# Kernel optimization log

Measured on AMD Instinct MI355X. Metric: run time of the kernel, lower is better.

Reference implementation:

```python
import jax, jax.numpy as jnp
import numpy as np

B, S, D_IN, D_OUT, H = 2, 2048, 1024, 1024, 16
HD = D_OUT // H

def setup_inputs() -> dict:
    key = jax.random.key(0)
    ks = jax.random.split(key, 6)
    sc = 1.0 / np.sqrt(D_IN)
    return {
        "x": jax.random.normal(ks[0], (B, S, D_IN), dtype=jnp.float32),
        "Wq": jax.random.normal(ks[1], (D_IN, D_OUT), dtype=jnp.float32) * sc,
        "Wk": jax.random.normal(ks[2], (D_IN, D_OUT), dtype=jnp.float32) * sc,
        "Wv": jax.random.normal(ks[3], (D_IN, D_OUT), dtype=jnp.float32) * sc,
        "Wo": jax.random.normal(ks[4], (D_OUT, D_OUT), dtype=jnp.float32) * (1.0 / np.sqrt(D_OUT)),
        "bo": jax.random.normal(ks[5], (D_OUT,), dtype=jnp.float32) * 0.01,
    }

def reference(x, Wq, Wk, Wv, Wo, bo):
    b, n, _ = x.shape
    # QKV projections -> [b, h, n, hd]
    def split_heads(t):
        return t.reshape(b, n, H, HD).transpose(0, 2, 1, 3)
    q = split_heads(x @ Wq)
    k = split_heads(x @ Wk)
    v = split_heads(x @ Wv)
    scores = jnp.einsum("bhqd,bhkd->bhqk", q, k) / jnp.sqrt(jnp.float32(HD))
    causal = jnp.tril(jnp.ones((n, n), dtype=bool))  # True = keep
    scores = jnp.where(causal[None, None], scores, -jnp.inf)
    attn = jax.nn.softmax(scores, axis=-1)
    ctx = jnp.einsum("bhqk,bhkd->bhqd", attn, v)  # [b,h,n,hd]
    ctx = ctx.transpose(0, 2, 1, 3).reshape(b, n, D_OUT)
    return ctx @ Wo + bo
```

## Files before the change

kernel.cpp:

```cpp
#include <hip/hip_runtime.h>

#define B_  2
#define S_  2048
#define D_  1024
#define H_  16
#define HD_ 64
#define M_  (B_*S_)

typedef __bf16 bf16_t;
typedef __bf16 bf16x8 __attribute__((ext_vector_type(8)));
typedef float  f32x4  __attribute__((ext_vector_type(4)));

union U16x8 { uint4 u; bf16x8 v; };
union U16x4 { uint2 u; bf16_t e[4]; };

__device__ __forceinline__ bf16x8 ld_frag(const bf16_t* p) {
    U16x8 t; t.u = *(const uint4*)p; return t.v;
}

__device__ __forceinline__ void gload16(const bf16_t* g, bf16_t* l) {
    __builtin_amdgcn_global_load_lds(
        (const __attribute__((address_space(1))) unsigned int*)g,
        (__attribute__((address_space(3))) unsigned int*)l,
        16, 0, 0);
}

__global__ __launch_bounds__(256) void ingest(const float* __restrict__ w0,
                                              const float* __restrict__ w1,
                                              const float* __restrict__ w2,
                                              const float* __restrict__ w3,
                                              const float* __restrict__ xin,
                                              bf16_t* __restrict__ wtout,
                                              bf16_t* __restrict__ xout) {
    const int RC = 1024;
    int z = blockIdx.z;
    if (z == 4) {
        int bid = blockIdx.y * 32 + blockIdx.x;
        int t = threadIdx.y * 32 + threadIdx.x;
        int i = bid * 4096 + t * 16;
#pragma unroll
        for (int g = 0; g < 2; g++) {
            float4 a = *(const float4*)(xin + i + g * 8);
            float4 b = *(const float4*)(xin + i + g * 8 + 4);
            bf16_t o[8] = {(bf16_t)a.x, (bf16_t)a.y, (bf16_t)a.z, (bf16_t)a.w,
                           (bf16_t)b.x, (bf16_t)b.y, (bf16_t)b.z, (bf16_t)b.w};
            *(uint4*)(xout + i + g * 8) = *(uint4*)o;
        }
        return;
    }
    __shared__ bf16_t tile[32][33];
    const float* in = (z == 0) ? w0 : (z == 1) ? w1 : (z == 2) ? w2 : w3;
    bf16_t* out = wtout + (size_t)z * RC * RC;
    int c0 = blockIdx.x * 32, r0 = blockIdx.y * 32;
    int tx = threadIdx.x, ty = threadIdx.y;
#pragma unroll
    for (int i = 0; i < 32; i += 8)
        tile[ty + i][tx] = (bf16_t)in[(size_t)(r0 + ty + i) * RC + c0 + tx];
    __syncthreads();
#pragma unroll
    for (int i = 0; i < 32; i += 8)
        out[(size_t)(c0 + ty + i) * RC + r0 + tx] = tile[tx][ty + i];
}

#define STAGE_TILE(A_, Wt_, koff, buf)                                        \
    _Pragma("unroll") for (int c = 0; c < 4; c++) {                           \
        int rb = c * 32 + wid * 8;                                            \
        gload16(A_  + arow + (size_t)rb * K + (koff), (buf) + rb * 64);       \
        gload16(Wt_ + brow + (size_t)rb * K + (koff), (buf) + 8192 + rb * 64);\
    }

#define GEMM_CORE(A_, Wt_)                                                    \
    const int K = 1024;                                                       \
    __shared__ __align__(16) bf16_t smem[32768];                              \
    int t = threadIdx.x;                                                      \
    int wid = t >> 6, lane = t & 63, ln = lane & 15, quad = lane >> 4;        \
    int wm = (wid >> 1) * 64, wn = (wid & 1) * 64;                            \
    f32x4 zero = {0.f, 0.f, 0.f, 0.f};                                        \
    f32x4 acc[4][4];                                                          \
    _Pragma("unroll") for (int i = 0; i < 4; i++)                             \
        _Pragma("unroll") for (int j = 0; j < 4; j++) acc[i][j] = zero;       \
    int sr8 = lane >> 3;                                                      \
    int scs = (((lane & 7) ^ sr8) * 8);              \
    int swr = (ln & 7) * 8;                          \
    const size_t arow = (size_t)(m0 + sr8) * K + scs;                         \
    const size_t brow = (size_t)(n0 + sr8) * K + scs;                         \
    STAGE_TILE(A_, Wt_, 0, smem)                                              \
    STAGE_TILE(A_, Wt_, 64, smem + 16384)                                     \
    for (int it = 0; it < 16; it++) {                                         \
        if (it < 15) asm volatile("s_waitcnt vmcnt(8)" ::: "memory");         \
        else         asm volatile("s_waitcnt vmcnt(0)" ::: "memory");         \
        __builtin_amdgcn_sched_barrier(0);                                    \
        __builtin_amdgcn_s_barrier();                                         \
        bf16_t* a_lds = smem + (it & 1) * 16384;                              \
        bf16_t* b_lds = a_lds + 8192;                                         \
        _Pragma("unroll") for (int ks = 0; ks < 2; ks++) {                    \
            bf16x8 af[4], bfr[4];                                             \
            _Pragma("unroll") for (int i = 0; i < 4; i++)                     \
                af[i] = ld_frag(a_lds + (wm + i * 16 + ln) * 64 +             \
                                ((ks * 32 + quad * 8) ^ swr));                \
            _Pragma("unroll") for (int j = 0; j < 4; j++)                     \
                bfr[j] = ld_frag(b_lds + (wn + j * 16 + ln) * 64 +            \
                                 ((ks * 32 + quad * 8) ^ swr));               \
            _Pragma("unroll") for (int i = 0; i < 4; i++)                     \
                _Pragma("unroll") for (int j = 0; j < 4; j++)                 \
                    acc[i][j] = __builtin_amdgcn_mfma_f32_16x16x32_bf16(      \
                        af[i], bfr[j], acc[i][j], 0, 0, 0);                   \
        }                                                                     \
        asm volatile("s_waitcnt lgkmcnt(0)" ::: "memory");                    \
        __builtin_amdgcn_sched_barrier(0);                                    \
        __builtin_amdgcn_s_barrier();                                         \
        if (it < 14) {                                                        \
            int koff = (it + 2) * 64;                                         \
            bf16_t* bufn = smem + (it & 1) * 16384;                           \
            STAGE_TILE(A_, Wt_, koff, bufn)                                   \
        }                                                                     \
    }

__global__ __launch_bounds__(256) void gemm_qkv(const bf16_t* __restrict__ A,
                                                const bf16_t* __restrict__ wtbase,
                                                bf16_t* __restrict__ outbase) {
    int wsel = blockIdx.x >> 3;
    int n0 = (blockIdx.x & 7) * 128;
    int m0 = blockIdx.y * 128;
    const bf16_t* Wt = wtbase + (size_t)wsel * 1024 * 1024;
    bf16_t* out = outbase + (size_t)wsel * 4 * 1024 * 1024;

    GEMM_CORE(A, Wt)

    if (wsel < 2) {
#pragma unroll
        for (int i = 0; i < 4; i++)
#pragma unroll
            for (int j = 0; j < 4; j++) {
                int n = n0 + wn + j * 16 + ln;
                int h = n >> 6, hd = n & 63;
#pragma unroll
                for (int r = 0; r < 4; r++) {
                    int m = m0 + wm + i * 16 + quad * 4 + r;
                    int b = m >> 11, s = m & 2047;
                    out[(((size_t)(b * H_ + h) * S_ + s) * HD_) + hd] =
                        (bf16_t)acc[i][j][r];
                }
            }
    } else {
        bf16_t* tr = smem;
#pragma unroll
        for (int i = 0; i < 4; i++)
#pragma unroll
            for (int j = 0; j < 4; j++) {
                U16x4 pk;
#pragma unroll
                for (int r = 0; r < 4; r++) pk.e[r] = (bf16_t)acc[i][j][r];
                *(uint2*)(tr + (wn + j * 16 + ln) * 136 + wm + i * 16 + quad * 4) = pk.u;
            }
        __syncthreads();
        int row = t >> 1, half = t & 1;
        int n = n0 + row;
        int h = n >> 6, hd = n & 63;
        int b = m0 >> 11, s0 = (m0 & 2047) + half * 64;
        const bf16_t* src = tr + row * 136 + half * 64;
        bf16_t* dst = out + (((size_t)(b * H_ + h) * HD_ + hd) * S_) + s0;
#pragma unroll
        for (int u = 0; u < 8; u++)
            *(uint4*)(dst + u * 8) = *(const uint4*)(src + u * 8);
    }
}

__global__ __launch_bounds__(256) void gemm_out(const bf16_t* __restrict__ A,
                                                const bf16_t* __restrict__ Wt,
                                                float* __restrict__ out,
                                                const float* __restrict__ bias) {
    const int N = 1024;
    int n0 = blockIdx.x * 128;
    int m0 = blockIdx.y * 128;

    GEMM_CORE(A, Wt)

#pragma unroll
    for (int i = 0; i < 4; i++)
#pragma unroll
        for (int j = 0; j < 4; j++) {
            int n = n0 + wn + j * 16 + ln;
            float bv = bias[n];
#pragma unroll
            for (int r = 0; r < 4; r++) {
                int m = m0 + wm + i * 16 + quad * 4 + r;
                out[(size_t)m * N + n] = acc[i][j][r] + bv;
            }
        }
}

__global__ __launch_bounds__(256) void attn64(const bf16_t* __restrict__ Q,
                                              const bf16_t* __restrict__ Kg,
                                              const bf16_t* __restrict__ Vt,
                                              bf16_t* __restrict__ ctx) {
    __shared__ __align__(16) bf16_t k_lds[64 * 72];
    __shared__ __align__(16) bf16_t v_lds[64 * 72];
    __shared__ __align__(16) bf16_t p_lds[4 * 16 * 72];

    int t = threadIdx.x;
    int wid = t >> 6, lane = t & 63, ln = lane & 15, quad = lane >> 4;

    int bid = blockIdx.x;
    int xcd = bid & 7, slot = bid >> 3;
    int bh  = xcd + ((slot >> 4) << 3);
    int pair = slot & 15;
    int b = bh >> 4, h = bh & 15;
    const bf16_t* Qb = Q  + (size_t)bh * S_ * HD_;
    const bf16_t* Kb = Kg + (size_t)bh * S_ * HD_;
    const bf16_t* Vb = Vt + (size_t)bh * HD_ * S_;

    int srow = t >> 2, schunk = t & 3;
    bf16_t* plw = p_lds + wid * 16 * 72;
    f32x4 zero = {0.f, 0.f, 0.f, 0.f};

    for (int pass = 0; pass < 2; pass++) {
        int qt = pass ? (31 - pair) : pair;
        int q0 = qt * 64;
        int nkt = qt + 1;

        int qrow = q0 + wid * 16 + ln;
        bf16x8 qf0 = ld_frag(Qb + (size_t)qrow * HD_ + quad * 8);
        bf16x8 qf1 = ld_frag(Qb + (size_t)qrow * HD_ + 32 + quad * 8);

        f32x4 oacc[4];
#pragma unroll
        for (int i = 0; i < 4; i++) oacc[i] = zero;
        float lsum[4] = {0.f, 0.f, 0.f, 0.f};

        const uint4* ksrc = (const uint4*)(Kb + (size_t)srow * HD_);
        const uint4* vsrc = (const uint4*)(Vb + (size_t)srow * S_);
        uint4 kv0 = ksrc[schunk * 2], kv1 = ksrc[schunk * 2 + 1];
        uint4 vv0 = vsrc[schunk * 2], vv1 = vsrc[schunk * 2 + 1];

        for (int kt = 0; kt < nkt; kt++) {
            __syncthreads();
            *(uint4*)(k_lds + srow * 72 + schunk * 16)     = kv0;
            *(uint4*)(k_lds + srow * 72 + schunk * 16 + 8) = kv1;
            *(uint4*)(v_lds + srow * 72 + schunk * 16)     = vv0;
            *(uint4*)(v_lds + srow * 72 + schunk * 16 + 8) = vv1;
            __syncthreads();
            if (kt + 1 < nkt) {
                int k0n = (kt + 1) * 64;
                ksrc = (const uint4*)(Kb + (size_t)(k0n + srow) * HD_);
                vsrc = (const uint4*)(Vb + (size_t)srow * S_ + k0n);
                kv0 = ksrc[schunk * 2]; kv1 = ksrc[schunk * 2 + 1];
                vv0 = vsrc[schunk * 2]; vv1 = vsrc[schunk * 2 + 1];
            }

            f32x4 sacc[4];
#pragma unroll
            for (int tt = 0; tt < 4; tt++) sacc[tt] = zero;
#pragma unroll
            for (int tt = 0; tt < 4; tt++) {
                bf16x8 b0 = ld_frag(k_lds + (tt * 16 + ln) * 72 + quad * 8);
                bf16x8 b1 = ld_frag(k_lds + (tt * 16 + ln) * 72 + 32 + quad * 8);
                sacc[tt] = __builtin_amdgcn_mfma_f32_16x16x32_bf16(qf0, b0, sacc[tt], 0, 0, 0);
                sacc[tt] = __builtin_amdgcn_mfma_f32_16x16x32_bf16(qf1, b1, sacc[tt], 0, 0, 0);
            }

            bool diag = (kt * 64 + 63 > q0 + wid * 16);
#pragma unroll
            for (int r = 0; r < 4; r++) {
                int q = q0 + wid * 16 + quad * 4 + r;
#pragma unroll
                for (int tt = 0; tt < 4; tt++) {
                    int k = kt * 64 + tt * 16 + ln;
                    float pv = __expf(__builtin_fmaf((float)sacc[tt][r], 0.125f, -16.0f));
                    if (diag && k > q) pv = 0.f;
                    lsum[r] += pv;
                    plw[(quad * 4 + r) * 72 + tt * 16 + ln] = (bf16_t)pv;
                }
            }

            bf16x8 pa0 = ld_frag(plw + ln * 72 + quad * 8);
            bf16x8 pa1 = ld_frag(plw + ln * 72 + 32 + quad * 8);
#pragma unroll
            for (int th = 0; th < 4; th++) {
                bf16x8 vb0 = ld_frag(v_lds + (th * 16 + ln) * 72 + quad * 8);
                bf16x8 vb1 = ld_frag(v_lds + (th * 16 + ln) * 72 + 32 + quad * 8);
                oacc[th] = __builtin_amdgcn_mfma_f32_16x16x32_bf16(pa0, vb0, oacc[th], 0, 0, 0);
                oacc[th] = __builtin_amdgcn_mfma_f32_16x16x32_bf16(pa1, vb1, oacc[th], 0, 0, 0);
            }
        }

#pragma unroll
        for (int r = 0; r < 4; r++) {
#pragma unroll
            for (int m = 1; m < 16; m <<= 1)
                lsum[r] += __shfl_xor(lsum[r], m, 64);
        }

#pragma unroll
        for (int r = 0; r < 4; r++) {
            int q = q0 + wid * 16 + quad * 4 + r;
            float inv = 1.f / lsum[r];
#pragma unroll
            for (int th = 0; th < 4; th++) {
                int hd = h * 64 + th * 16 + ln;
                ctx[((size_t)(b * S_ + q)) * D_ + hd] = (bf16_t)(oacc[th][r] * inv);
            }
        }
    }
}

extern "C" void kernel_launch(void* const* d_in, const int* in_sizes, int n_in,
                              void* d_out, int out_size, void* d_ws, size_t ws_size,
                              hipStream_t stream) {
    const float* x  = (const float*)d_in[0];
    const float* bo = (const float*)d_in[5];
    float* out = (float*)d_out;

    bf16_t* ws = (bf16_t*)d_ws;
    const size_t MM = 1024 * 1024;
    bf16_t* xb  = ws;
    bf16_t* ctx = xb;
    bf16_t* wtq = xb + 4 * MM;
    bf16_t* wto = wtq + 3 * MM;
    bf16_t* qb  = wto + MM;
    bf16_t* kb  = qb + 4 * MM;
    bf16_t* vtb = kb + 4 * MM;

    ingest<<<dim3(32, 32, 5), dim3(32, 8, 1), 0, stream>>>(
        (const float*)d_in[1], (const float*)d_in[2],
        (const float*)d_in[3], (const float*)d_in[4], x, wtq, xb);

    gemm_qkv<<<dim3(24, 32, 1), 256, 0, stream>>>(xb, wtq, qb);

    attn64<<<512, 256, 0, stream>>>(qb, kb, vtb, ctx);

    gemm_out<<<dim3(8, 32, 1), 256, 0, stream>>>(ctx, wto, out, bo);
}
```

Before: 198.3 us.

## Compute S transposed so P stays in registers for PV MFMA

Swaps the MFMA operands in the QK^T product so each lane holds scores for its own query column. The exponentiated probabilities can then feed straight into 16x16x16 bf16 MFMAs as the A operand, without a round trip through LDS. This drops the p_lds buffer, its stores and reloads, and shrinks the row-sum reduction to two shuffles. In exchange the PV product uses twice as many smaller MFMAs and narrower 8-byte V loads from LDS.

```diff
diff --git a/kernel.cpp b/kernel.cpp
--- a/kernel.cpp
+++ b/kernel.cpp
@@ -10,9 +10,11 @@
 typedef __bf16 bf16_t;
 typedef __bf16 bf16x8 __attribute__((ext_vector_type(8)));
 typedef float  f32x4  __attribute__((ext_vector_type(4)));
+typedef short  s16x4  __attribute__((ext_vector_type(4)));
 
 union U16x8 { uint4 u; bf16x8 v; };
 union U16x4 { uint2 u; bf16_t e[4]; };
+union U16x4s { uint2 u; s16x4 s; bf16_t e[4]; };
 
 __device__ __forceinline__ bf16x8 ld_frag(const bf16_t* p) {
     U16x8 t; t.u = *(const uint4*)p; return t.v;
@@ -108,7 +110,7 @@
         }                                                                     \
         asm volatile("s_waitcnt lgkmcnt(0)" ::: "memory");                    \
         __builtin_amdgcn_sched_barrier(0);                                    \
-        __builtin_amdgcn_s_barrier();                                         \
+        __builtin_amdgcn_s_barrier();                                        \
         if (it < 14) {                                                        \
             int koff = (it + 2) * 64;                                         \
             bf16_t* bufn = smem + (it & 1) * 16384;                           \
@@ -196,7 +198,6 @@
                                               bf16_t* __restrict__ ctx) {
     __shared__ __align__(16) bf16_t k_lds[64 * 72];
     __shared__ __align__(16) bf16_t v_lds[64 * 72];
-    __shared__ __align__(16) bf16_t p_lds[4 * 16 * 72];
 
     int t = threadIdx.x;
     int wid = t >> 6, lane = t & 63, ln = lane & 15, quad = lane >> 4;
@@ -211,7 +212,6 @@
     const bf16_t* Vb = Vt + (size_t)bh * HD_ * S_;
 
     int srow = t >> 2, schunk = t & 3;
-    bf16_t* plw = p_lds + wid * 16 * 72;
     f32x4 zero = {0.f, 0.f, 0.f, 0.f};
 
     for (int pass = 0; pass < 2; pass++) {
@@ -226,7 +226,7 @@
         f32x4 oacc[4];
 #pragma unroll
         for (int i = 0; i < 4; i++) oacc[i] = zero;
-        float lsum[4] = {0.f, 0.f, 0.f, 0.f};
+        float lsum = 0.f;
 
         const uint4* ksrc = (const uint4*)(Kb + (size_t)srow * HD_);
         const uint4* vsrc = (const uint4*)(Vb + (size_t)srow * S_);
@@ -253,48 +253,46 @@
             for (int tt = 0; tt < 4; tt++) sacc[tt] = zero;
 #pragma unroll
             for (int tt = 0; tt < 4; tt++) {
-                bf16x8 b0 = ld_frag(k_lds + (tt * 16 + ln) * 72 + quad * 8);
-                bf16x8 b1 = ld_frag(k_lds + (tt * 16 + ln) * 72 + 32 + quad * 8);
-                sacc[tt] = __builtin_amdgcn_mfma_f32_16x16x32_bf16(qf0, b0, sacc[tt], 0, 0, 0);
-                sacc[tt] = __builtin_amdgcn_mfma_f32_16x16x32_bf16(qf1, b1, sacc[tt], 0, 0, 0);
+                bf16x8 a0 = ld_frag(k_lds + (tt * 16 + ln) * 72 + quad * 8);
+                bf16x8 a1 = ld_frag(k_lds + (tt * 16 + ln) * 72 + 32 + quad * 8);
+                sacc[tt] = __builtin_amdgcn_mfma_f32_16x16x32_bf16(a0, qf0, sacc[tt], 0, 0, 0);
+                sacc[tt] = __builtin_amdgcn_mfma_f32_16x16x32_bf16(a1, qf1, sacc[tt], 0, 0, 0);
             }
 
             bool diag = (kt * 64 + 63 > q0 + wid * 16);
-#pragma unroll
-            for (int r = 0; r < 4; r++) {
-                int q = q0 + wid * 16 + quad * 4 + r;
+            U16x4s pa[4];
+#pragma unroll
+            for (int tt = 0; tt < 4; tt++) {
+#pragma unroll
+                for (int r = 0; r < 4; r++) {
+                    int kg = kt * 64 + tt * 16 + quad * 4 + r;
+                    float pv = __expf(__builtin_fmaf((float)sacc[tt][r], 0.125f, -16.0f));
+                    if (diag && kg > qrow) pv = 0.f;
+                    lsum += pv;
+                    pa[tt].e[r] = (bf16_t)pv;
+                }
+            }
+
+#pragma unroll
+            for (int th = 0; th < 4; th++) {
 #pragma unroll
                 for (int tt = 0; tt < 4; tt++) {
-                    int k = kt * 64 + tt * 16 + ln;
-                    float pv = __expf(__builtin_fmaf((float)sacc[tt][r], 0.125f, -16.0f));
-                    if (diag && k > q) pv = 0.f;
-                    lsum[r] += pv;
-                    plw[(quad * 4 + r) * 72 + tt * 16 + ln] = (bf16_t)pv;
+                    U16x4s vb;
+                    vb.u = *(const uint2*)(v_lds + (th * 16 + ln) * 72 +
+                                           tt * 16 + quad * 4);
+                    oacc[th] = __builtin_amdgcn_mfma_f32_16x16x16bf16_1k(
+                        pa[tt].s, vb.s, oacc[th], 0, 0, 0);
                 }
             }
-
-            bf16x8 pa0 = ld_frag(plw + ln * 72 + quad * 8);
-            bf16x8 pa1 = ld_frag(plw + ln * 72 + 32 + quad * 8);
-#pragma unroll
-            for (int th = 0; th < 4; th++) {
-                bf16x8 vb0 = ld_frag(v_lds + (th * 16 + ln) * 72 + quad * 8);
-                bf16x8 vb1 = ld_frag(v_lds + (th * 16 + ln) * 72 + 32 + quad * 8);
-                oacc[th] = __builtin_amdgcn_mfma_f32_16x16x32_bf16(pa0, vb0, oacc[th], 0, 0, 0);
-                oacc[th] = __builtin_amdgcn_mfma_f32_16x16x32_bf16(pa1, vb1, oacc[th], 0, 0, 0);
-            }
         }
 
-#pragma unroll
-        for (int r = 0; r < 4; r++) {
-#pragma unroll
-            for (int m = 1; m < 16; m <<= 1)
-                lsum[r] += __shfl_xor(lsum[r], m, 64);
-        }
+        lsum += __shfl_xor(lsum, 16);
+        lsum += __shfl_xor(lsum, 32);
 
 #pragma unroll
         for (int r = 0; r < 4; r++) {
             int q = q0 + wid * 16 + quad * 4 + r;
-            float inv = 1.f / lsum[r];
+            float inv = 1.f / __shfl(lsum, quad * 4 + r);
 #pragma unroll
             for (int th = 0; th < 4; th++) {
                 int hd = h * 64 + th * 16 + ln;
```

Result: no change. 197.2 us (-0.6%).
